# Optimization experiments

Measured on AMD Instinct MI355X. Metric: run time of the kernel, lower is better.

## Reference

```python
import jax, jax.numpy as jnp
import numpy as np


def _local2d(x, weight, stride, padding):
    """Locally-connected 2D conv: per-output-location filters.
    x: [N, C, H, W], weight: [h_out, w_out, O, C, k, k].
    Returns [N, O, h_out, w_out].
    """
    h_out, w_out, O, C, k, _ = weight.shape
    if padding > 0:
        x = jnp.pad(x, ((0, 0), (0, 0), (padding, padding), (padding, padding)))
    # Gather all k x k windows at once (no python loop over locations).
    ih = (jnp.arange(h_out) * stride)[:, None] + jnp.arange(k)[None, :]  # [h_out, k]
    iw = (jnp.arange(w_out) * stride)[:, None] + jnp.arange(k)[None, :]  # [w_out, k]
    # patches: [N, C, h_out, w_out, k, k]
    patches = x[:, :, ih[:, None, :, None], iw[None, :, None, :]]
    # out[n,o,h,w] = sum_{c,p,q} weight[h,w,o,c,p,q] * patches[n,c,h,w,p,q]
    return jnp.einsum('hwocpq,nchwpq->nohw', weight, patches)


def setup_inputs() -> dict:
    key = jax.random.key(0)
    k1, k2 = jax.random.split(key)
    B, CAT, C, H, W = 32, 10, 32, 32, 32
    O, K, STRIDE, PAD = 64, 3, 1, 1
    h_out = (H + 2 * PAD - K) // STRIDE + 1
    w_out = (W + 2 * PAD - K) // STRIDE + 1
    x = jax.random.normal(k1, (B, CAT, C, H, W), dtype=jnp.float32)
    # init_local with first_layer=False, mono=False: std = 1/sqrt(0.5*C*K^2)
    std = 1.0 / np.sqrt(0.5 * C * K ** 2)
    weight = jax.random.normal(k2, (h_out, w_out, O, C, K, K), dtype=jnp.float32) * std
    bias = jnp.zeros((CAT, O, h_out, w_out), dtype=jnp.float32)
    return {"x": x, "weight": weight, "bias": bias}


def reference(x, weight, bias):
    STRIDE, PAD = 1, 1
    B, CAT = x.shape[:2]
    x_flat = x.reshape((B * CAT,) + x.shape[2:])            # [B*CAT, C, H, W]
    out_flat = _local2d(x_flat, weight, STRIDE, PAD)        # [B*CAT, O, h_out, w_out]
    out = out_flat.reshape((B, CAT) + out_flat.shape[1:])   # [B, CAT, O, h_out, w_out]
    return out + bias[None]
```

## Files before the change

### kernel.cpp

```cpp
#include <hip/hip_runtime.h>
#include <hip/hip_bf16.h>


typedef __attribute__((ext_vector_type(8))) short short8;
typedef __attribute__((ext_vector_type(4))) float f32x4;
typedef __attribute__((ext_vector_type(4))) unsigned short ushort4b;

#define XT2_ELEMS 10485760
#define ZSLAB_ELEMS 10240
#define OUTS_OFF_BYTES 20992000

__device__ __forceinline__ unsigned short f2bf(float f) {
    __hip_bfloat16 b = __float2bfloat16(f);
    return __builtin_bit_cast(unsigned short, b);
}

__global__ __launch_bounds__(256) void VecLocal2d_xpose(const float* __restrict__ x,
                                                        unsigned short* __restrict__ xT2) {
    __shared__ unsigned short tile[64][68];
    if (blockIdx.x == 0) {
#pragma unroll
        for (int j = 0; j < 20; ++j)
            reinterpret_cast<unsigned int*>(xT2 + XT2_ELEMS)[threadIdx.x + j * 256] = 0u;
    }
    const int mcb = blockIdx.x >> 4;
    const int yxb = blockIdx.x & 15;
    const int t = threadIdx.x;
    const int g = t >> 4;
    const int l4 = (t & 15) * 4;
#pragma unroll
    for (int p = 0; p < 4; ++p) {
        const int ml = g + p * 16;
        const float4 v = *reinterpret_cast<const float4*>(
            x + (size_t)(mcb * 64 + ml) * 1024 + yxb * 64 + l4);
        ushort4b u;
        u.x = f2bf(v.x); u.y = f2bf(v.y); u.z = f2bf(v.z); u.w = f2bf(v.w);
        *reinterpret_cast<ushort4b*>(&tile[ml][l4]) = u;
    }
    __syncthreads();
#pragma unroll
    for (int p = 0; p < 4; ++p) {
        const int yl = g + p * 16;
        ushort4b u;
        u.x = tile[l4 + 0][yl];
        u.y = tile[l4 + 1][yl];
        u.z = tile[l4 + 2][yl];
        u.w = tile[l4 + 3][yl];
        *reinterpret_cast<ushort4b*>(xT2 + (size_t)(yxb * 64 + yl) * 10240 + mcb * 64 + l4) = u;
    }
}

__global__ __launch_bounds__(256, 4) void VecLocal2d_main(const unsigned short* __restrict__ xT2,
                                                          const float* __restrict__ weight,
                                                          float* __restrict__ out_s) {
    __shared__ unsigned short wLDS[64 * 296];

    const int bid = blockIdx.x;
    const int s = bid >> 7;
    const int hg = bid & 127;
    const int h = hg >> 2;
    const int w = ((hg & 3) << 3) | s;
    const int loc = h * 32 + w;

    const int tid = threadIdx.x;
    const int lane = tid & 63;
    const int wave = tid >> 6;
    const int quad = lane >> 4;
    const int l16 = lane & 15;
    const int wm = wave >> 1, wn = wave & 1;

    const float* wg = weight + (size_t)loc * 18432;
#pragma unroll
    for (int i = 0; i < 18; ++i) {
        const int f4i = tid + i * 256;
        const float4 v = reinterpret_cast<const float4*>(wg)[f4i];
        const int o = f4i / 72;
        const int kbase = (f4i - o * 72) * 4;
        const float vv[4] = {v.x, v.y, v.z, v.w};
#pragma unroll
        for (int e = 0; e < 4; ++e) {
            const int k = kbase + e;
            const int c = k / 9;
            const int r = k - c * 9;
            wLDS[o * 296 + r * 32 + c] = f2bf(vv[e]);
        }
    }

    int base[9];
#pragma unroll
    for (int dy = 0; dy < 3; ++dy)
#pragma unroll
        for (int dx = 0; dx < 3; ++dx) {
            const int y = h - 1 + dy;
            const int xc = w - 1 + dx;
            const bool valid = ((unsigned)y < 32u) && ((unsigned)xc < 32u);
            base[dy * 3 + dx] = valid ? (y * 32 + xc) * 10240 : XT2_ELEMS;
        }

    __syncthreads();

    short8 bfr[2][9];
#pragma unroll
    for (int tni = 0; tni < 2; ++tni) {
        const int o = (wn * 2 + tni) * 16 + l16;
#pragma unroll
        for (int kt = 0; kt < 9; ++kt)
            bfr[tni][kt] = *reinterpret_cast<const short8*>(&wLDS[o * 296 + kt * 32 + quad * 8]);
    }

    const int laneA = (wm * 32 + l16) * 32 + quad * 8;
    float* os = out_s + (size_t)loc * 20480;

    for (int mt = 0; mt < 5; ++mt) {
        const int moff = laneA + mt * 2048;
        f32x4 acc[2][2] = {};
#pragma unroll
        for (int kt = 0; kt < 9; ++kt) {
            const short8 a0 = *reinterpret_cast<const short8*>(xT2 + base[kt] + moff);
            const short8 a1 = *reinterpret_cast<const short8*>(xT2 + base[kt] + moff + 512);
            acc[0][0] = __builtin_amdgcn_mfma_f32_16x16x32_bf16(a0, bfr[0][kt], acc[0][0], 0, 0, 0);
            acc[0][1] = __builtin_amdgcn_mfma_f32_16x16x32_bf16(a0, bfr[1][kt], acc[0][1], 0, 0, 0);
            acc[1][0] = __builtin_amdgcn_mfma_f32_16x16x32_bf16(a1, bfr[0][kt], acc[1][0], 0, 0, 0);
            acc[1][1] = __builtin_amdgcn_mfma_f32_16x16x32_bf16(a1, bfr[1][kt], acc[1][1], 0, 0, 0);
        }

#pragma unroll
        for (int tmi = 0; tmi < 2; ++tmi)
#pragma unroll
            for (int tni = 0; tni < 2; ++tni) {
                const int o = (wn * 2 + tni) * 16 + l16;
#pragma unroll
                for (int r = 0; r < 4; ++r) {
                    const int m = mt * 64 + (wm * 2 + tmi) * 16 + quad * 4 + r;
                    os[m * 64 + o] = acc[tmi][tni][r];
                }
            }
    }
}

__global__ __launch_bounds__(256) void VecLocal2d_outT(const float* __restrict__ out_s,
                                                       const float* __restrict__ bias,
                                                       float* __restrict__ out) {
    __shared__ float tile[64][65];
    const int m = blockIdx.x >> 4;
    const int loc0 = (blockIdx.x & 15) * 64;
    const int t = threadIdx.x;
    const float* src = out_s + (size_t)loc0 * 20480 + m * 64;
#pragma unroll
    for (int p = 0; p < 4; ++p) {
        const int idx = p * 256 + t;
        const int lr = idx >> 4;
        const int c4 = (idx & 15) * 4;
        const float4 v = *reinterpret_cast<const float4*>(src + (size_t)lr * 20480 + c4);
        tile[lr][c4 + 0] = v.x; tile[lr][c4 + 1] = v.y;
        tile[lr][c4 + 2] = v.z; tile[lr][c4 + 3] = v.w;
    }
    __syncthreads();
    const int cat = m % 10;
#pragma unroll
    for (int p = 0; p < 4; ++p) {
        const int idx = p * 256 + t;
        const int o = idx >> 4;
        const int l4 = (idx & 15) * 4;
        const float4 bv = *reinterpret_cast<const float4*>(
            bias + ((size_t)(cat * 64 + o)) * 1024 + loc0 + l4);
        float4 v;
        v.x = tile[l4 + 0][o] + bv.x;
        v.y = tile[l4 + 1][o] + bv.y;
        v.z = tile[l4 + 2][o] + bv.z;
        v.w = tile[l4 + 3][o] + bv.w;
        *reinterpret_cast<float4*>(out + ((size_t)(m * 64 + o)) * 1024 + loc0 + l4) = v;
    }
}

extern "C" void kernel_launch(void* const* d_in, const int* in_sizes, int n_in,
                              void* d_out, int out_size, void* d_ws, size_t ws_size,
                              hipStream_t stream) {
    const float* x = (const float*)d_in[0];
    const float* wgt = (const float*)d_in[1];
    const float* bias = (const float*)d_in[2];
    float* out = (float*)d_out;
    unsigned short* xT2 = (unsigned short*)d_ws;
    float* out_s = (float*)((char*)d_ws + OUTS_OFF_BYTES);

    VecLocal2d_xpose<<<2560, 256, 0, stream>>>(x, xT2);
    VecLocal2d_main<<<1024, 256, 0, stream>>>(xT2, wgt, out_s);
    VecLocal2d_outT<<<5120, 256, 0, stream>>>(out_s, bias, out);
}
```

Measured before the change: 222.9 us.

## Prepack bf16 weights in prep kernel and store intermediate output as bf16

```diff
diff --git a/kernel.cpp b/kernel.cpp
--- a/kernel.cpp
+++ b/kernel.cpp
@@ -8,53 +8,88 @@
 
 #define XT2_ELEMS 10485760
 #define ZSLAB_ELEMS 10240
-#define OUTS_OFF_BYTES 20992000
+#define WP_OFF_BYTES 20992000
+#define OUTS_OFF_BYTES 58740736
 
 __device__ __forceinline__ unsigned short f2bf(float f) {
     __hip_bfloat16 b = __float2bfloat16(f);
     return __builtin_bit_cast(unsigned short, b);
 }
-
-__global__ __launch_bounds__(256) void VecLocal2d_xpose(const float* __restrict__ x,
-                                                        unsigned short* __restrict__ xT2) {
-    __shared__ unsigned short tile[64][68];
-    if (blockIdx.x == 0) {
-#pragma unroll
-        for (int j = 0; j < 20; ++j)
-            reinterpret_cast<unsigned int*>(xT2 + XT2_ELEMS)[threadIdx.x + j * 256] = 0u;
-    }
-    const int mcb = blockIdx.x >> 4;
-    const int yxb = blockIdx.x & 15;
+__device__ __forceinline__ float bf2f(unsigned short u) {
+    unsigned int v = ((unsigned int)u) << 16;
+    return __builtin_bit_cast(float, v);
+}
+
+__global__ __launch_bounds__(256) void VecLocal2d_prep(const float* __restrict__ x,
+                                                       const float* __restrict__ wgt,
+                                                       unsigned short* __restrict__ xT2,
+                                                       unsigned short* __restrict__ wP) {
+    __shared__ unsigned short lds[18432];
+    const int b = blockIdx.x;
     const int t = threadIdx.x;
-    const int g = t >> 4;
-    const int l4 = (t & 15) * 4;
-#pragma unroll
-    for (int p = 0; p < 4; ++p) {
-        const int ml = g + p * 16;
-        const float4 v = *reinterpret_cast<const float4*>(
-            x + (size_t)(mcb * 64 + ml) * 1024 + yxb * 64 + l4);
-        ushort4b u;
-        u.x = f2bf(v.x); u.y = f2bf(v.y); u.z = f2bf(v.z); u.w = f2bf(v.w);
-        *reinterpret_cast<ushort4b*>(&tile[ml][l4]) = u;
-    }
-    __syncthreads();
-#pragma unroll
-    for (int p = 0; p < 4; ++p) {
-        const int yl = g + p * 16;
-        ushort4b u;
-        u.x = tile[l4 + 0][yl];
-        u.y = tile[l4 + 1][yl];
-        u.z = tile[l4 + 2][yl];
-        u.w = tile[l4 + 3][yl];
-        *reinterpret_cast<ushort4b*>(xT2 + (size_t)(yxb * 64 + yl) * 10240 + mcb * 64 + l4) = u;
+    if (b < 2560) {
+        unsigned short (*tile)[68] = (unsigned short(*)[68])lds;
+        if (b == 0) {
+#pragma unroll
+            for (int j = 0; j < 20; ++j)
+                reinterpret_cast<unsigned int*>(xT2 + XT2_ELEMS)[t + j * 256] = 0u;
+        }
+        const int mcb = b >> 4;
+        const int yxb = b & 15;
+        const int g = t >> 4;
+        const int l4 = (t & 15) * 4;
+#pragma unroll
+        for (int p = 0; p < 4; ++p) {
+            const int ml = g + p * 16;
+            const float4 v = *reinterpret_cast<const float4*>(
+                x + (size_t)(mcb * 64 + ml) * 1024 + yxb * 64 + l4);
+            ushort4b u;
+            u.x = f2bf(v.x); u.y = f2bf(v.y); u.z = f2bf(v.z); u.w = f2bf(v.w);
+            *reinterpret_cast<ushort4b*>(&tile[ml][l4]) = u;
+        }
+        __syncthreads();
+#pragma unroll
+        for (int p = 0; p < 4; ++p) {
+            const int yl = g + p * 16;
+            ushort4b u;
+            u.x = tile[l4 + 0][yl];
+            u.y = tile[l4 + 1][yl];
+            u.z = tile[l4 + 2][yl];
+            u.w = tile[l4 + 3][yl];
+            *reinterpret_cast<ushort4b*>(xT2 + (size_t)(yxb * 64 + yl) * 10240 + mcb * 64 + l4) = u;
+        }
+    } else {
+        const int loc = b - 2560;
+        const float* wg = wgt + (size_t)loc * 18432;
+#pragma unroll
+        for (int i = 0; i < 18; ++i) {
+            const int f4i = t + i * 256;
+            const float4 v = reinterpret_cast<const float4*>(wg)[f4i];
+            const float vv[4] = {v.x, v.y, v.z, v.w};
+#pragma unroll
+            for (int e = 0; e < 4; ++e) {
+                const int klin = f4i * 4 + e;
+                const int o = klin / 288;
+                const int rem = klin - o * 288;
+                const int c = rem / 9;
+                const int r = rem - c * 9;
+                lds[((r * 4 + (c >> 3)) * 64 + o) * 8 + (c & 7)] = f2bf(vv[e]);
+            }
+        }
+        __syncthreads();
+        unsigned short* wp = wP + (size_t)loc * 18432;
+#pragma unroll
+        for (int i = 0; i < 9; ++i) {
+            const int idx = t + i * 256;
+            *reinterpret_cast<short8*>(wp + idx * 8) =
+                *reinterpret_cast<const short8*>(&lds[idx * 8]);
+        }
     }
 }
 
 __global__ __launch_bounds__(256, 4) void VecLocal2d_main(const unsigned short* __restrict__ xT2,
-                                                          const float* __restrict__ weight,
-                                                          float* __restrict__ out_s) {
-    __shared__ unsigned short wLDS[64 * 296];
-
+                                                          const unsigned short* __restrict__ wP,
+                                                          unsigned short* __restrict__ out_s) {
     const int bid = blockIdx.x;
     const int s = bid >> 7;
     const int hg = bid & 127;
@@ -67,23 +102,17 @@
     const int wave = tid >> 6;
     const int quad = lane >> 4;
     const int l16 = lane & 15;
-    const int wm = wave >> 1, wn = wave & 1;
-
-    const float* wg = weight + (size_t)loc * 18432;
-#pragma unroll
-    for (int i = 0; i < 18; ++i) {
-        const int f4i = tid + i * 256;
-        const float4 v = reinterpret_cast<const float4*>(wg)[f4i];
-        const int o = f4i / 72;
-        const int kbase = (f4i - o * 72) * 4;
-        const float vv[4] = {v.x, v.y, v.z, v.w};
-#pragma unroll
-        for (int e = 0; e < 4; ++e) {
-            const int k = kbase + e;
-            const int c = k / 9;
-            const int r = k - c * 9;
-            wLDS[o * 296 + r * 32 + c] = f2bf(vv[e]);
-        }
+    const int wm = wave >> 1, wo = wave & 1;
+
+    const unsigned short* wloc = wP + (size_t)loc * 18432;
+    short8 bfr[2][9];
+#pragma unroll
+    for (int oi = 0; oi < 2; ++oi) {
+        const int o = (wo * 2 + oi) * 16 + l16;
+#pragma unroll
+        for (int kt = 0; kt < 9; ++kt)
+            bfr[oi][kt] = *reinterpret_cast<const short8*>(
+                wloc + ((kt * 4 + quad) * 64 + o) * 8);
     }
 
     int base[9];
@@ -97,79 +126,72 @@
             base[dy * 3 + dx] = valid ? (y * 32 + xc) * 10240 : XT2_ELEMS;
         }
 
-    __syncthreads();
-
-    short8 bfr[2][9];
-#pragma unroll
-    for (int tni = 0; tni < 2; ++tni) {
-        const int o = (wn * 2 + tni) * 16 + l16;
-#pragma unroll
-        for (int kt = 0; kt < 9; ++kt)
-            bfr[tni][kt] = *reinterpret_cast<const short8*>(&wLDS[o * 296 + kt * 32 + quad * 8]);
-    }
-
-    const int laneA = (wm * 32 + l16) * 32 + quad * 8;
-    float* os = out_s + (size_t)loc * 20480;
+    const int laneB = l16 * 32 + quad * 8;
+    unsigned short* os = out_s + (size_t)loc * 20480;
 
     for (int mt = 0; mt < 5; ++mt) {
-        const int moff = laneA + mt * 2048;
+        const int m0 = (mt * 64 + wm * 32) * 32 + laneB;
         f32x4 acc[2][2] = {};
 #pragma unroll
         for (int kt = 0; kt < 9; ++kt) {
-            const short8 a0 = *reinterpret_cast<const short8*>(xT2 + base[kt] + moff);
-            const short8 a1 = *reinterpret_cast<const short8*>(xT2 + base[kt] + moff + 512);
-            acc[0][0] = __builtin_amdgcn_mfma_f32_16x16x32_bf16(a0, bfr[0][kt], acc[0][0], 0, 0, 0);
-            acc[0][1] = __builtin_amdgcn_mfma_f32_16x16x32_bf16(a0, bfr[1][kt], acc[0][1], 0, 0, 0);
-            acc[1][0] = __builtin_amdgcn_mfma_f32_16x16x32_bf16(a1, bfr[0][kt], acc[1][0], 0, 0, 0);
-            acc[1][1] = __builtin_amdgcn_mfma_f32_16x16x32_bf16(a1, bfr[1][kt], acc[1][1], 0, 0, 0);
-        }
-
-#pragma unroll
-        for (int tmi = 0; tmi < 2; ++tmi)
-#pragma unroll
-            for (int tni = 0; tni < 2; ++tni) {
-                const int o = (wn * 2 + tni) * 16 + l16;
+            const short8 p0 = *reinterpret_cast<const short8*>(xT2 + base[kt] + m0);
+            const short8 p1 = *reinterpret_cast<const short8*>(xT2 + base[kt] + m0 + 512);
+            acc[0][0] = __builtin_amdgcn_mfma_f32_16x16x32_bf16(bfr[0][kt], p0, acc[0][0], 0, 0, 0);
+            acc[0][1] = __builtin_amdgcn_mfma_f32_16x16x32_bf16(bfr[0][kt], p1, acc[0][1], 0, 0, 0);
+            acc[1][0] = __builtin_amdgcn_mfma_f32_16x16x32_bf16(bfr[1][kt], p0, acc[1][0], 0, 0, 0);
+            acc[1][1] = __builtin_amdgcn_mfma_f32_16x16x32_bf16(bfr[1][kt], p1, acc[1][1], 0, 0, 0);
+        }
+#pragma unroll
+        for (int oi = 0; oi < 2; ++oi)
+#pragma unroll
+            for (int mi = 0; mi < 2; ++mi) {
+                const int m = mt * 64 + wm * 32 + mi * 16 + l16;
 #pragma unroll
                 for (int r = 0; r < 4; ++r) {
-                    const int m = mt * 64 + (wm * 2 + tmi) * 16 + quad * 4 + r;
-                    os[m * 64 + o] = acc[tmi][tni][r];
+                    const int o = (wo * 2 + oi) * 16 + quad * 4 + r;
+                    os[o * 320 + m] = f2bf(acc[oi][mi][r]);
                 }
             }
     }
 }
 
-__global__ __launch_bounds__(256) void VecLocal2d_outT(const float* __restrict__ out_s,
+__global__ __launch_bounds__(256) void VecLocal2d_outT(const unsigned short* __restrict__ out_s,
                                                        const float* __restrict__ bias,
                                                        float* __restrict__ out) {
-    __shared__ float tile[64][65];
-    const int m = blockIdx.x >> 4;
-    const int loc0 = (blockIdx.x & 15) * 64;
+    __shared__ float tile[64][68];
+    const int b = blockIdx.x;
+    const int o = b & 63;
+    const int mtlt = b >> 6;
+    const int mt = mtlt >> 4;
+    const int lt = mtlt & 15;
     const int t = threadIdx.x;
-    const float* src = out_s + (size_t)loc0 * 20480 + m * 64;
-#pragma unroll
-    for (int p = 0; p < 4; ++p) {
-        const int idx = p * 256 + t;
-        const int lr = idx >> 4;
-        const int c4 = (idx & 15) * 4;
-        const float4 v = *reinterpret_cast<const float4*>(src + (size_t)lr * 20480 + c4);
-        tile[lr][c4 + 0] = v.x; tile[lr][c4 + 1] = v.y;
-        tile[lr][c4 + 2] = v.z; tile[lr][c4 + 3] = v.w;
+    const int lr = t >> 2;
+    const int q = t & 3;
+    const unsigned short* src =
+        out_s + (size_t)(lt * 64 + lr) * 20480 + o * 320 + mt * 64 + q * 16;
+    const short8 v0 = *reinterpret_cast<const short8*>(src);
+    const short8 v1 = *reinterpret_cast<const short8*>(src + 8);
+#pragma unroll
+    for (int j = 0; j < 8; ++j) {
+        tile[q * 16 + j][lr] = bf2f((unsigned short)v0[j]);
+        tile[q * 16 + 8 + j][lr] = bf2f((unsigned short)v1[j]);
     }
     __syncthreads();
+    const int ml = t >> 2;
+    const int lq = t & 3;
+    const int m = mt * 64 + ml;
     const int cat = m % 10;
-#pragma unroll
-    for (int p = 0; p < 4; ++p) {
-        const int idx = p * 256 + t;
-        const int o = idx >> 4;
-        const int l4 = (idx & 15) * 4;
-        const float4 bv = *reinterpret_cast<const float4*>(
-            bias + ((size_t)(cat * 64 + o)) * 1024 + loc0 + l4);
+    const float* bp = bias + ((size_t)(cat * 64 + o)) * 1024 + lt * 64 + lq * 16;
+    float* op = out + ((size_t)(m * 64 + o)) * 1024 + lt * 64 + lq * 16;
+#pragma unroll
+    for (int j = 0; j < 4; ++j) {
+        const float4 bv = *reinterpret_cast<const float4*>(bp + j * 4);
         float4 v;
-        v.x = tile[l4 + 0][o] + bv.x;
-        v.y = tile[l4 + 1][o] + bv.y;
-        v.z = tile[l4 + 2][o] + bv.z;
-        v.w = tile[l4 + 3][o] + bv.w;
-        *reinterpret_cast<float4*>(out + ((size_t)(m * 64 + o)) * 1024 + loc0 + l4) = v;
+        v.x = tile[ml][lq * 16 + j * 4 + 0] + bv.x;
+        v.y = tile[ml][lq * 16 + j * 4 + 1] + bv.y;
+        v.z = tile[ml][lq * 16 + j * 4 + 2] + bv.z;
+        v.w = tile[ml][lq * 16 + j * 4 + 3] + bv.w;
+        *reinterpret_cast<float4*>(op + j * 4) = v;
     }
 }
 
@@ -181,9 +203,10 @@
     const float* bias = (const float*)d_in[2];
     float* out = (float*)d_out;
     unsigned short* xT2 = (unsigned short*)d_ws;
-    float* out_s = (float*)((char*)d_ws + OUTS_OFF_BYTES);
-
-    VecLocal2d_xpose<<<2560, 256, 0, stream>>>(x, xT2);
-    VecLocal2d_main<<<1024, 256, 0, stream>>>(xT2, wgt, out_s);
+    unsigned short* wP = (unsigned short*)((char*)d_ws + WP_OFF_BYTES);
+    unsigned short* out_s = (unsigned short*)((char*)d_ws + OUTS_OFF_BYTES);
+
+    VecLocal2d_prep<<<3584, 256, 0, stream>>>(x, wgt, xT2, wP);
+    VecLocal2d_main<<<1024, 256, 0, stream>>>(xT2, wP, out_s);
     VecLocal2d_outT<<<5120, 256, 0, stream>>>(out_s, bias, out);
 }
```

Result: slower. 253.6 us (+13.8%).
